# Performance work log

Measured on AMD Instinct MI355X. Metric: run time of the kernel, lower is better.

The kernel has to match this reference:

```python
import jax, jax.numpy as jnp
import numpy as np
from jax import lax

B, T, MEL, D, H, NC = 8, 256, 128, 192, 4, 20
C_EVENT, C_SCENE = 8, 64
ETA, LR, ALPHA = 0.9, 0.1, 0.01  # memory momentum, write lr, forget rate
EPS = 1e-5


def _ln(x, g, b):
    m = x.mean(-1, keepdims=True)
    v = ((x - m) ** 2).mean(-1, keepdims=True)
    return (x - m) / jnp.sqrt(v + EPS) * g + b


def _mem_step(x, t, M, S, Wk, Wv, Wq, chunk):
    # x: [B,D]; M,S: [B,D,D]. Titans-style neural memory, updated every `chunk` steps.
    k = x @ Wk
    v = x @ Wv
    q = x @ Wq
    err = v - jnp.einsum('bd,bde->be', k, M)          # surprise / prediction error
    S_new = ETA * S + LR * jnp.einsum('bd,be->bde', k, err)
    M_new = (1.0 - ALPHA) * M + S_new
    upd = (t % chunk) == 0
    S = jnp.where(upd, S_new, S)
    M = jnp.where(upd, M_new, M)
    out = jnp.einsum('bd,bde->be', q, M)              # retrieval
    return out, M, S


def setup_inputs() -> dict:
    key = jax.random.key(0)
    ks = jax.random.split(key, 24)
    w = lambda k, shp, s=0.05: jax.random.normal(k, shp, dtype=jnp.float32) * s
    inp = {
        'x': jax.random.normal(ks[0], (B, T, MEL), dtype=jnp.float32),
        'W_in': w(ks[1], (MEL, D)), 'b_in': jnp.zeros((D,), jnp.float32),
        # MHA at seq_len=1: softmax over one key -> weight 1, so only V and out proj matter
        'Wv_a': w(ks[2], (D, D)), 'bv_a': jnp.zeros((D,), jnp.float32),
        'Wo_a': w(ks[3], (D, D)), 'bo_a': jnp.zeros((D,), jnp.float32),
        # conformer conv module (degenerate seq_len=1: depthwise conv -> center tap)
        'ln1_g': jnp.ones((D,), jnp.float32), 'ln1_b': jnp.zeros((D,), jnp.float32),
        'pw1_w': w(ks[4], (D, 2 * D)), 'pw1_b': jnp.zeros((2 * D,), jnp.float32),
        'dw_w': w(ks[5], (D,), 0.2), 'dw_b': jnp.zeros((D,), jnp.float32),
        'bn_s': jnp.ones((D,), jnp.float32), 'bn_b': jnp.zeros((D,), jnp.float32),
        'pw2_w': w(ks[6], (D, D)), 'pw2_b': jnp.zeros((D,), jnp.float32),
        # theta (event) / delta (scene) neural memory projections
        'Wk_t': w(ks[7], (D, D)), 'Wv_t': w(ks[8], (D, D)), 'Wq_t': w(ks[9], (D, D)),
        'Wk_d': w(ks[10], (D, D)), 'Wv_d': w(ks[11], (D, D)), 'Wq_d': w(ks[12], (D, D)),
        'ln2_g': jnp.ones((D,), jnp.float32), 'ln2_b': jnp.zeros((D,), jnp.float32),
        'Wc': w(ks[13], (D, NC)), 'bc': jnp.zeros((NC,), jnp.float32),
    }
    return inp


def reference(x, W_in, b_in, Wv_a, bv_a, Wo_a, bo_a, ln1_g, ln1_b, pw1_w, pw1_b,
              dw_w, dw_b, bn_s, bn_b, pw2_w, pw2_b, Wk_t, Wv_t, Wq_t,
              Wk_d, Wv_d, Wq_d, ln2_g, ln2_b, Wc, bc):
    xp = x @ W_in + b_in                               # [B,T,D]

    def step(carry, inp):
        x_t, t = inp                                   # x_t: [B,D]
        Mt, St, Md, Sd = carry
        d_out, Md, Sd = _mem_step(x_t, t, Md, Sd, Wk_d, Wv_d, Wq_d, C_SCENE)
        x1 = x_t + 0.5 * d_out
        attn = (x1 @ Wv_a + bv_a) @ Wo_a + bo_a        # single-token self-attn
        x2 = x1 + attn
        h = _ln(x2, ln1_g, ln1_b)
        h = h @ pw1_w + pw1_b
        a, g = jnp.split(h, 2, axis=-1)
        h = a * jax.nn.sigmoid(g)                      # GLU
        h = h * dw_w + dw_b                            # depthwise conv center tap
        h = h * bn_s + bn_b                            # eval-mode BN
        h = jax.nn.silu(h)
        h = h @ pw2_w + pw2_b
        x3 = x2 + h
        t_out, Mt, St = _mem_step(x3, t, Mt, St, Wk_t, Wv_t, Wq_t, C_EVENT)
        x4 = x3 + 0.5 * t_out
        return (Mt, St, Md, Sd), _ln(x4, ln2_g, ln2_b)

    z = jnp.zeros((B, D, D), jnp.float32)
    xs = (jnp.swapaxes(xp, 0, 1), jnp.arange(T))       # [T,B,D], [T]
    _, ys = lax.scan(step, (z, z, z, z), xs)
    y = jnp.swapaxes(ys, 0, 1)                         # [B,T,D]
    pooled = y.mean(axis=1)
    return pooled @ Wc + bc                            # [B,NC]
```

## Files before the change

kernel.cpp:

```cpp
#include <hip/hip_runtime.h>
#include <math.h>

#define Bb 8
#define Tt 256
#define MEL 128
#define Dd 192
#define NCc 20
#define ND 4
#define NT 32
#define ETAc 0.9f
#define LRc 0.1f
#define MDEC 0.99f
#define EPSc 1e-5f
#define PT 4
#define RTT 8
#define PADD 196
#define UPAD 193

__device__ __forceinline__ float sigmoidf_(float x) {
    return 1.0f / (1.0f + __expf(-x));
}

__device__ __forceinline__ float memcoef(int n, int i) {
    float m = LRc, pw = LRc;
    for (int nn = i + 1; nn <= n; nn++) { pw *= ETAc; m = MDEC * m + pw; }
    return m;
}

__device__ __forceinline__ float dot4(float4 a, float4 b) {
    return a.x * b.x + a.y * b.y + a.z * b.z + a.w * b.w;
}

__global__ __launch_bounds__(192) void setup(
    const float* __restrict__ Wv_a, const float* __restrict__ Wo_a,
    const float* __restrict__ bv_a, const float* __restrict__ bo_a,
    const float* __restrict__ Wq_t, const float* __restrict__ Wq_d,
    const float* __restrict__ x, const float* __restrict__ W_in,
    const float* __restrict__ b_in, const float* __restrict__ Wk_d,
    const float* __restrict__ Wv_d,
    float* __restrict__ Wavo_ws, float* __restrict__ b_avo,
    float* __restrict__ WqtT, float* __restrict__ WqdT,
    float* __restrict__ Kd_ws, float* __restrict__ Vd_ws,
    float* __restrict__ pooled, unsigned int* __restrict__ ctr)
{
    __shared__ __align__(16) float smem[512];
    int blk = blockIdx.x, tid = threadIdx.x;

    if (blk < 192) {
        int m = blk;
        smem[tid] = Wv_a[m * Dd + tid];
        __syncthreads();
        int o = tid;
        float acc = 0.f;
        #pragma unroll 8
        for (int k = 0; k < Dd; k += 4) {
            acc += Wo_a[(k + 0) * Dd + o] * smem[k + 0];
            acc += Wo_a[(k + 1) * Dd + o] * smem[k + 1];
            acc += Wo_a[(k + 2) * Dd + o] * smem[k + 2];
            acc += Wo_a[(k + 3) * Dd + o] * smem[k + 3];
        }
        Wavo_ws[m * Dd + o] = acc;
        return;
    }
    if (blk == 192) {
        int o = tid;
        float s = bo_a[o];
        #pragma unroll 4
        for (int m = 0; m < Dd; m++) s += bv_a[m] * Wo_a[m * Dd + o];
        b_avo[o] = s;
        return;
    }
    if (blk < 241) {
        int r0 = 4 * (blk - 193);
        float4 v;
        v.x = Wq_t[(r0 + 0) * Dd + tid];
        v.y = Wq_t[(r0 + 1) * Dd + tid];
        v.z = Wq_t[(r0 + 2) * Dd + tid];
        v.w = Wq_t[(r0 + 3) * Dd + tid];
        *(float4*)&WqtT[tid * Dd + r0] = v;
        return;
    }
    if (blk < 289) {
        int r0 = 4 * (blk - 241);
        float4 v;
        v.x = Wq_d[(r0 + 0) * Dd + tid];
        v.y = Wq_d[(r0 + 1) * Dd + tid];
        v.z = Wq_d[(r0 + 2) * Dd + tid];
        v.w = Wq_d[(r0 + 3) * Dd + tid];
        *(float4*)&WqdT[tid * Dd + r0] = v;
        return;
    }
    if (blk == 289) {
        for (int q = tid; q < Bb * Dd; q += 192) pooled[q] = 0.f;
        if (tid == 0) *ctr = 0u;
        return;
    }

    int q = blk - 290;
    int b = q >> 2, i = q & 3;
    float* XR = smem;
    float* XP = smem + 128;
    if (tid < 128) XR[tid] = x[((size_t)b * Tt + 64 * i) * MEL + tid];
    __syncthreads();
    {
        int o = tid;
        float acc = b_in[o];
        #pragma unroll 8
        for (int k = 0; k < MEL; k += 4) {
            acc += W_in[(k + 0) * Dd + o] * XR[k + 0];
            acc += W_in[(k + 1) * Dd + o] * XR[k + 1];
            acc += W_in[(k + 2) * Dd + o] * XR[k + 2];
            acc += W_in[(k + 3) * Dd + o] * XR[k + 3];
        }
        XP[o] = acc;
    }
    __syncthreads();
    {
        int o = tid;
        float ak = 0.f, av = 0.f;
        #pragma unroll 4
        for (int k = 0; k < Dd; k += 4) {
            float x0 = XP[k + 0], x1 = XP[k + 1], x2 = XP[k + 2], x3 = XP[k + 3];
            ak += Wk_d[(k + 0) * Dd + o] * x0 + Wk_d[(k + 1) * Dd + o] * x1
                + Wk_d[(k + 2) * Dd + o] * x2 + Wk_d[(k + 3) * Dd + o] * x3;
            av += Wv_d[(k + 0) * Dd + o] * x0 + Wv_d[(k + 1) * Dd + o] * x1
                + Wv_d[(k + 2) * Dd + o] * x2 + Wv_d[(k + 3) * Dd + o] * x3;
        }
        Kd_ws[(b * ND + i) * Dd + o] = ak;
        Vd_ws[(b * ND + i) * Dd + o] = av;
    }
}

__global__ __launch_bounds__(192) void delta_solve(
    const float* __restrict__ WqdT, const float* __restrict__ Kd_ws,
    float* __restrict__ Vd_ws, float* __restrict__ Ud_ws)
{
    int blk = blockIdx.x, b = blk / 5, role = blk % 5, tid = threadIdx.x;
    if (role == 0) {
        __shared__ __align__(16) float K4[ND][Dd], V4[ND][Dd];
        __shared__ float G[16], mc[16];
        for (int q = tid; q < ND * 48; q += 192) {
            int i = q / 48, c = q - i * 48;
            ((float4*)K4[i])[c] = ((const float4*)&Kd_ws[(b * ND + i) * Dd])[c];
            ((float4*)V4[i])[c] = ((const float4*)&Vd_ws[(b * ND + i) * Dd])[c];
        }
        __syncthreads();
        if (tid < 16) {
            int i = tid >> 2, j = tid & 3;
            float s = 0.f;
            for (int d = 0; d < Dd; d++) s += K4[i][d] * K4[j][d];
            G[tid] = s;
            mc[tid] = (j <= i) ? memcoef(i, j) : 0.f;
        }
        __syncthreads();
        for (int i = 1; i < ND; i++) {
            float acc = V4[i][tid];
            for (int m = 0; m < i; m++)
                acc -= mc[(i - 1) * ND + m] * G[i * ND + m] * V4[m][tid];
            V4[i][tid] = acc;
        }
        for (int i = 0; i < ND; i++) Vd_ws[(b * ND + i) * Dd + tid] = V4[i][tid];
    } else {
        __shared__ float KS[Dd];
        int i = role - 1;
        KS[tid] = Kd_ws[(b * ND + i) * Dd + tid];
        __syncthreads();
        int o = tid;
        float acc = 0.f;
        #pragma unroll 8
        for (int k = 0; k < Dd; k += 4) {
            acc += WqdT[(k + 0) * Dd + o] * KS[k + 0];
            acc += WqdT[(k + 1) * Dd + o] * KS[k + 1];
            acc += WqdT[(k + 2) * Dd + o] * KS[k + 2];
            acc += WqdT[(k + 3) * Dd + o] * KS[k + 3];
        }
        Ud_ws[(b * ND + i) * Dd + o] = acc;
    }
}

__global__ __launch_bounds__(192) void pipeline(
    const float* __restrict__ x, const float* __restrict__ W_in,
    const float* __restrict__ b_in,
    const float* __restrict__ ln1_g, const float* __restrict__ ln1_b,
    const float* __restrict__ pw1_w, const float* __restrict__ pw1_b,
    const float* __restrict__ dw_w, const float* __restrict__ dw_b,
    const float* __restrict__ bn_s, const float* __restrict__ bn_b,
    const float* __restrict__ pw2_w, const float* __restrict__ pw2_b,
    const float* __restrict__ Wavo_ws, const float* __restrict__ b_avo,
    const float* __restrict__ Ed_ws, const float* __restrict__ Ud_ws,
    const float* __restrict__ Wk_t, const float* __restrict__ Wv_t,
    const float* __restrict__ WqtT,
    float* __restrict__ x3_ws, float* __restrict__ Kt_ws,
    float* __restrict__ Vt_ws, float* __restrict__ Ut_ws)
{
    int blk = blockIdx.x;
    int b = blk >> 6, tile = blk & 63;
    int t0 = tile * PT, n = tile >> 4;
    int tid = threadIdx.x;

    __shared__ __align__(16) float XR[PT][MEL];
    __shared__ __align__(16) float XP[PT][Dd];
    __shared__ __align__(16) float ED[ND][PADD], UD[ND][PADD];
    __shared__ __align__(16) float X1[PT][Dd], X2[PT][Dd];
    __shared__ __align__(16) float LNX[PT][Dd], HG[PT][Dd];
    __shared__ float X3row[Dd];
    __shared__ float KTs[Dd];
    __shared__ float WQs[PT * ND];
    __shared__ float mv[PT][2];

    if (tid < 128) {
        int r = tid >> 5, c = tid & 31;
        ((float4*)XR[r])[c] = ((const float4*)&x[((size_t)b * Tt + t0 + r) * MEL])[c];
    }
    for (int q = tid; q < ND * 48 * 2; q += 192) {
        int which = q >= ND * 48;
        int qq = which ? q - ND * 48 : q;
        int i = qq / 48, c = qq - i * 48;
        if (!which) ((float4*)ED[i])[c] = ((const float4*)&Ed_ws[(b * ND + i) * Dd])[c];
        else        ((float4*)UD[i])[c] = ((const float4*)&Ud_ws[(b * ND + i) * Dd])[c];
    }
    __syncthreads();

    int o = tid;
    {
        float acc[PT];
        float bb = b_in[o];
        #pragma unroll
        for (int r = 0; r < PT; r++) acc[r] = bb;
        #pragma unroll 8
        for (int k = 0; k < MEL; k += 4) {
            float w0 = W_in[(k + 0) * Dd + o], w1 = W_in[(k + 1) * Dd + o];
            float w2 = W_in[(k + 2) * Dd + o], w3 = W_in[(k + 3) * Dd + o];
            #pragma unroll
            for (int r = 0; r < PT; r++) {
                float4 xv = *(const float4*)&XR[r][k];
                acc[r] += w0 * xv.x + w1 * xv.y + w2 * xv.z + w3 * xv.w;
            }
        }
        #pragma unroll
        for (int r = 0; r < PT; r++) XP[r][tid] = acc[r];
    }
    __syncthreads();

    if (tid < 128) {
        int r = tid >> 5, i = (tid >> 3) & 3, c = tid & 7;
        float s = 0.f;
        const float* xp = XP[r];
        const float* u = UD[i];
        #pragma unroll
        for (int j = 0; j < 24; j++) s += xp[c * 24 + j] * u[c * 24 + j];
        s += __shfl_down(s, 4, 8);
        s += __shfl_down(s, 2, 8);
        s += __shfl_down(s, 1, 8);
        if (c == 0) {
            float coef = (i <= n) ? memcoef(n, i) : 0.f;
            WQs[r * ND + i] = s * coef;
        }
    }
    __syncthreads();

    {
        #pragma unroll
        for (int r = 0; r < PT; r++) {
            float dout = WQs[r * ND + 0] * ED[0][tid] + WQs[r * ND + 1] * ED[1][tid]
                       + WQs[r * ND + 2] * ED[2][tid] + WQs[r * ND + 3] * ED[3][tid];
            X1[r][tid] = XP[r][tid] + 0.5f * dout;
        }
    }
    __syncthreads();

    {
        float acc[PT];
        float bb = b_avo[o];
        #pragma unroll
        for (int r = 0; r < PT; r++) acc[r] = bb;
        #pragma unroll 8
        for (int k = 0; k < Dd; k += 4) {
            float w0 = Wavo_ws[(k + 0) * Dd + o], w1 = Wavo_ws[(k + 1) * Dd + o];
            float w2 = Wavo_ws[(k + 2) * Dd + o], w3 = Wavo_ws[(k + 3) * Dd + o];
            #pragma unroll
            for (int r = 0; r < PT; r++) {
                float4 xv = *(const float4*)&X1[r][k];
                acc[r] += w0 * xv.x + w1 * xv.y + w2 * xv.z + w3 * xv.w;
            }
        }
        #pragma unroll
        for (int r = 0; r < PT; r++) X2[r][tid] = X1[r][tid] + acc[r];
    }
    __syncthreads();

    if (tid < 128) {
        int r = tid >> 5, j = tid & 31;
        float s = 0.f, sq = 0.f;
        for (int d = j; d < Dd; d += 32) { float v = X2[r][d]; s += v; sq += v * v; }
        for (int off = 16; off > 0; off >>= 1) {
            s += __shfl_down(s, off, 32); sq += __shfl_down(sq, off, 32);
        }
        if (j == 0) {
            float mean = s / Dd;
            mv[r][0] = mean;
            mv[r][1] = rsqrtf(sq / Dd - mean * mean + EPSc);
        }
    }
    __syncthreads();
    {
        float g = ln1_g[tid], bb = ln1_b[tid];
        #pragma unroll
        for (int r = 0; r < PT; r++)
            LNX[r][tid] = (X2[r][tid] - mv[r][0]) * mv[r][1] * g + bb;
    }
    __syncthreads();

    {
        float aa[PT], gg[PT];
        float ba = pw1_b[o], bg = pw1_b[o + Dd];
        #pragma unroll
        for (int r = 0; r < PT; r++) { aa[r] = ba; gg[r] = bg; }
        #pragma unroll 4
        for (int k = 0; k < Dd; k += 4) {
            float wa0 = pw1_w[(k + 0) * 2 * Dd + o], wg0 = pw1_w[(k + 0) * 2 * Dd + Dd + o];
            float wa1 = pw1_w[(k + 1) * 2 * Dd + o], wg1 = pw1_w[(k + 1) * 2 * Dd + Dd + o];
            float wa2 = pw1_w[(k + 2) * 2 * Dd + o], wg2 = pw1_w[(k + 2) * 2 * Dd + Dd + o];
            float wa3 = pw1_w[(k + 3) * 2 * Dd + o], wg3 = pw1_w[(k + 3) * 2 * Dd + Dd + o];
            #pragma unroll
            for (int r = 0; r < PT; r++) {
                float4 xv = *(const float4*)&LNX[r][k];
                aa[r] += wa0 * xv.x + wa1 * xv.y + wa2 * xv.z + wa3 * xv.w;
                gg[r] += wg0 * xv.x + wg1 * xv.y + wg2 * xv.z + wg3 * xv.w;
            }
        }
        float dww = dw_w[o], dwb = dw_b[o], bns = bn_s[o], bnb = bn_b[o];
        #pragma unroll
        for (int r = 0; r < PT; r++) {
            float h = aa[r] * sigmoidf_(gg[r]);
            h = h * dww + dwb;
            h = h * bns + bnb;
            h = h * sigmoidf_(h);
            HG[r][tid] = h;
        }
    }
    __syncthreads();

    {
        float acc[PT];
        float bb = pw2_b[o];
        #pragma unroll
        for (int r = 0; r < PT; r++) acc[r] = bb;
        #pragma unroll 8
        for (int k = 0; k < Dd; k += 4) {
            float w0 = pw2_w[(k + 0) * Dd + o], w1 = pw2_w[(k + 1) * Dd + o];
            float w2 = pw2_w[(k + 2) * Dd + o], w3 = pw2_w[(k + 3) * Dd + o];
            #pragma unroll
            for (int r = 0; r < PT; r++) {
                float4 xv = *(const float4*)&HG[r][k];
                acc[r] += w0 * xv.x + w1 * xv.y + w2 * xv.z + w3 * xv.w;
            }
        }
        #pragma unroll
        for (int r = 0; r < PT; r++) {
            float v = X2[r][tid] + acc[r];
            if (r == 0) X3row[tid] = v;
            x3_ws[((size_t)b * Tt + t0 + r) * Dd + tid] = v;
        }
    }

    if ((tile & 1) == 0) {
        int i8 = tile >> 1;
        __syncthreads();
        {
            float ak = 0.f, av = 0.f;
            #pragma unroll 4
            for (int k = 0; k < Dd; k += 4) {
                float x0 = X3row[k + 0], x1v = X3row[k + 1];
                float x2v = X3row[k + 2], x3v = X3row[k + 3];
                ak += Wk_t[(k + 0) * Dd + o] * x0 + Wk_t[(k + 1) * Dd + o] * x1v
                    + Wk_t[(k + 2) * Dd + o] * x2v + Wk_t[(k + 3) * Dd + o] * x3v;
                av += Wv_t[(k + 0) * Dd + o] * x0 + Wv_t[(k + 1) * Dd + o] * x1v
                    + Wv_t[(k + 2) * Dd + o] * x2v + Wv_t[(k + 3) * Dd + o] * x3v;
            }
            Kt_ws[(b * NT + i8) * Dd + o] = ak;
            Vt_ws[(b * NT + i8) * Dd + o] = av;
            KTs[o] = ak;
        }
        __syncthreads();
        {
            float au = 0.f;
            #pragma unroll 8
            for (int k = 0; k < Dd; k += 4) {
                au += WqtT[(k + 0) * Dd + o] * KTs[k + 0]
                    + WqtT[(k + 1) * Dd + o] * KTs[k + 1]
                    + WqtT[(k + 2) * Dd + o] * KTs[k + 2]
                    + WqtT[(k + 3) * Dd + o] * KTs[k + 3];
            }
            Ut_ws[(b * NT + i8) * Dd + o] = au;
        }
    }
}

__global__ __launch_bounds__(192) void theta_solve(
    const float* __restrict__ Kt_ws, const float* __restrict__ Vt_ws,
    float* __restrict__ Et_ws)
{
    int b = blockIdx.x, tid = threadIdx.x;
    __shared__ __align__(16) float K[NT][PADD], V[NT][PADD];
    __shared__ float G[NT * NT], mcc[NT * NT];
    __shared__ float T[NT * 33];

    for (int q = tid; q < NT * 48; q += 192) {
        int i = q / 48, c = q - i * 48;
        ((float4*)K[i])[c] = ((const float4*)&Kt_ws[(b * NT + i) * Dd])[c];
        ((float4*)V[i])[c] = ((const float4*)&Vt_ws[(b * NT + i) * Dd])[c];
    }
    if (tid < NT) {
        int i = tid;
        float m = 0.f, pw = LRc;
        for (int nn = 0; nn < NT; nn++) {
            float v;
            if (nn < i) v = 0.f;
            else if (nn == i) { m = LRc; v = m; }
            else { pw *= ETAc; m = MDEC * m + pw; v = m; }
            mcc[nn * NT + i] = v;
        }
    }
    __syncthreads();
    for (int p = tid; p < NT * NT; p += 192) {
        int i = p >> 5, j = p & 31;
        const float4* ki = (const float4*)K[i];
        const float4* kj = (const float4*)K[j];
        float s = 0.f;
        #pragma unroll 4
        for (int kk = 0; kk < 48; kk++) s += dot4(ki[kk], kj[kk]);
        G[p] = s;
    }
    __syncthreads();
    for (int p = tid; p < NT * NT; p += 192) {
        int i = p >> 5, m = p & 31;
        G[p] = (m < i) ? mcc[(i - 1) * NT + m] * G[p] : 0.f;
    }
    __syncthreads();
    if (tid < NT) {
        int j = tid;
        T[j * 33 + j] = 1.f;
        for (int i = j + 1; i < NT; i++) {
            float s = 0.f;
            for (int m = j; m < i; m++) s += G[i * NT + m] * T[m * 33 + j];
            T[i * 33 + j] = -s;
        }
    }
    __syncthreads();
    {
        for (int i = 0; i < NT; i++) {
            float s = 0.f;
            for (int j = 0; j <= i; j++) s += T[i * 33 + j] * V[j][tid];
            Et_ws[(b * NT + i) * Dd + tid] = s;
        }
    }
}

__global__ __launch_bounds__(256) void retrieve(
    const float* __restrict__ x3_ws, const float* __restrict__ Ut_ws,
    const float* __restrict__ Et_ws, const float* __restrict__ ln2_g,
    const float* __restrict__ ln2_b, float* __restrict__ pooled,
    const float* __restrict__ Wc, const float* __restrict__ bc,
    float* __restrict__ out, unsigned int* __restrict__ ctr)
{
    int blk = blockIdx.x, b = blk >> 5, tile = blk & 31;
    int t0 = tile * RTT, n = tile;
    int tid = threadIdx.x;

    __shared__ float UT[NT][UPAD];
    __shared__ __align__(16) float XS[RTT][PADD];
    __shared__ float WQ[RTT * NT];
    __shared__ float mv[RTT][2];
    __shared__ float PLD[Bb * Dd];
    __shared__ bool isLast;

    for (int q = tid; q < NT * Dd; q += 256) {
        int i = q / Dd, c = q - i * Dd;
        UT[i][c] = Ut_ws[(size_t)b * NT * Dd + q];
    }
    for (int q = tid; q < RTT * 48; q += 256) {
        int r = q / 48, c = q - r * 48;
        ((float4*)XS[r])[c] = ((const float4*)&x3_ws[((size_t)b * Tt + t0 + r) * Dd])[c];
    }
    __syncthreads();

    {
        int r = tid >> 5, i = tid & 31;
        const float* u = UT[i];
        const float* xr = XS[r];
        float s = 0.f;
        #pragma unroll 8
        for (int kk = 0; kk < Dd; kk++) s += u[kk] * xr[kk];
        float coef = (i <= n) ? memcoef(n, i) : 0.f;
        WQ[tid] = s * coef;
    }
    __syncthreads();

    if (tid < Dd) {
        float acc[RTT] = {};
        #pragma unroll 4
        for (int i = 0; i < NT; i++) {
            float e = Et_ws[(b * NT + i) * Dd + tid];
            #pragma unroll
            for (int r = 0; r < RTT; r++) acc[r] += WQ[r * NT + i] * e;
        }
        #pragma unroll
        for (int r = 0; r < RTT; r++) XS[r][tid] += 0.5f * acc[r];
    }
    __syncthreads();

    {
        int r = tid >> 5, j = tid & 31;
        float s = 0.f, sq = 0.f;
        for (int d = j; d < Dd; d += 32) { float v = XS[r][d]; s += v; sq += v * v; }
        for (int off = 16; off > 0; off >>= 1) {
            s += __shfl_down(s, off, 32); sq += __shfl_down(sq, off, 32);
        }
        if (j == 0) {
            float mean = s / Dd;
            mv[r][0] = mean;
            mv[r][1] = rsqrtf(sq / Dd - mean * mean + EPSc);
        }
    }
    __syncthreads();

    if (tid < Dd) {
        float g = ln2_g[tid], bb = ln2_b[tid];
        float sum = 0.f;
        #pragma unroll
        for (int r = 0; r < RTT; r++)
            sum += (XS[r][tid] - mv[r][0]) * mv[r][1] * g + bb;
        atomicAdd(&pooled[b * Dd + tid], sum);
    }

    __threadfence();
    if (tid == 0) {
        unsigned int old = atomicAdd(ctr, 1u);
        isLast = (old == (unsigned)(Bb * 32 - 1));
    }
    __syncthreads();
    if (isLast) {
        __threadfence();
        for (int q = tid; q < Bb * Dd; q += 256)
            PLD[q] = *(volatile const float*)&pooled[q];
        __syncthreads();
        if (tid < Bb * NCc) {
            int bo = tid / NCc, c = tid - bo * NCc;
            float s = 0.f;
            for (int d = 0; d < Dd; d++) s += PLD[bo * Dd + d] * Wc[d * NCc + c];
            out[tid] = s * (1.0f / Tt) + bc[c];
        }
    }
}

extern "C" void kernel_launch(void* const* d_in, const int* in_sizes, int n_in,
                              void* d_out, int out_size, void* d_ws, size_t ws_size,
                              hipStream_t stream) {
    const float* x     = (const float*)d_in[0];
    const float* W_in  = (const float*)d_in[1];
    const float* b_in  = (const float*)d_in[2];
    const float* Wv_a  = (const float*)d_in[3];
    const float* bv_a  = (const float*)d_in[4];
    const float* Wo_a  = (const float*)d_in[5];
    const float* bo_a  = (const float*)d_in[6];
    const float* ln1_g = (const float*)d_in[7];
    const float* ln1_b = (const float*)d_in[8];
    const float* pw1_w = (const float*)d_in[9];
    const float* pw1_b = (const float*)d_in[10];
    const float* dw_w  = (const float*)d_in[11];
    const float* dw_b  = (const float*)d_in[12];
    const float* bn_s  = (const float*)d_in[13];
    const float* bn_b  = (const float*)d_in[14];
    const float* pw2_w = (const float*)d_in[15];
    const float* pw2_b = (const float*)d_in[16];
    const float* Wk_t  = (const float*)d_in[17];
    const float* Wv_t  = (const float*)d_in[18];
    const float* Wq_t  = (const float*)d_in[19];
    const float* Wk_d  = (const float*)d_in[20];
    const float* Wv_d  = (const float*)d_in[21];
    const float* Wq_d  = (const float*)d_in[22];
    const float* ln2_g = (const float*)d_in[23];
    const float* ln2_b = (const float*)d_in[24];
    const float* Wc    = (const float*)d_in[25];
    const float* bc    = (const float*)d_in[26];

    float* ws = (float*)d_ws;
    size_t off = 0;
    float* x3_ws   = ws + off; off += (size_t)Bb * Tt * Dd;
    float* Kd_ws   = ws + off; off += Bb * ND * Dd;
    float* Vd_ws   = ws + off; off += Bb * ND * Dd;
    float* Ud_ws   = ws + off; off += Bb * ND * Dd;
    float* Kt_ws   = ws + off; off += Bb * NT * Dd;
    float* Vt_ws   = ws + off; off += Bb * NT * Dd;
    float* Et_ws   = ws + off; off += Bb * NT * Dd;
    float* Ut_ws   = ws + off; off += Bb * NT * Dd;
    float* pooled  = ws + off; off += Bb * Dd;
    float* Wavo_ws = ws + off; off += Dd * Dd;
    float* WqtT    = ws + off; off += Dd * Dd;
    float* WqdT    = ws + off; off += Dd * Dd;
    float* b_avo   = ws + off; off += Dd;
    unsigned int* ctr = (unsigned int*)(ws + off); off += 1;

    setup<<<322, 192, 0, stream>>>(
        Wv_a, Wo_a, bv_a, bo_a, Wq_t, Wq_d,
        x, W_in, b_in, Wk_d, Wv_d,
        Wavo_ws, b_avo, WqtT, WqdT, Kd_ws, Vd_ws, pooled, ctr);
    delta_solve<<<Bb * 5, 192, 0, stream>>>(WqdT, Kd_ws, Vd_ws, Ud_ws);
    pipeline<<<Bb * 64, 192, 0, stream>>>(
        x, W_in, b_in, ln1_g, ln1_b, pw1_w, pw1_b, dw_w, dw_b,
        bn_s, bn_b, pw2_w, pw2_b, Wavo_ws, b_avo, Vd_ws, Ud_ws,
        Wk_t, Wv_t, WqtT, x3_ws, Kt_ws, Vt_ws, Ut_ws);
    theta_solve<<<Bb, 192, 0, stream>>>(Kt_ws, Vt_ws, Et_ws);
    retrieve<<<Bb * 32, 256, 0, stream>>>(
        x3_ws, Ut_ws, Et_ws, ln2_g, ln2_b, pooled, Wc, bc, (float*)d_out, ctr);
}
```

Baseline: 224.7 us.

## Fold delta and theta solves into preceding kernels via last-block atomic counters

Removes the separate delta_solve and theta_solve launches. The last-arriving block of setup, and the last block per batch of pipeline, now does the solve work using atomic counters and threadfences. The Ut projection moves from per-tile pipeline blocks into the theta solve block as a batched 32-row matmul, and pipeline shared memory is unioned. This cuts launch overhead and dependency gaps, but serializes the delta solve for all 8 batches onto one block and adds a hipMemsetAsync for the counters.

```diff
diff --git a/kernel.cpp b/kernel.cpp
--- a/kernel.cpp
+++ b/kernel.cpp
@@ -41,36 +41,39 @@
     float* __restrict__ Wavo_ws, float* __restrict__ b_avo,
     float* __restrict__ WqtT, float* __restrict__ WqdT,
     float* __restrict__ Kd_ws, float* __restrict__ Vd_ws,
-    float* __restrict__ pooled, unsigned int* __restrict__ ctr)
+    float* __restrict__ Ud_ws,
+    float* __restrict__ pooled, unsigned int* __restrict__ ctrs)
 {
-    __shared__ __align__(16) float smem[512];
+    __shared__ __align__(16) float scol[Dd];
+    __shared__ __align__(16) float XR[MEL];
+    __shared__ __align__(16) float XPs[Dd];
+    __shared__ __align__(16) float TK[ND][Dd], TV[ND][Dd];
+    __shared__ float TG[16], TMC[16];
+    __shared__ bool lastFlag;
+
     int blk = blockIdx.x, tid = threadIdx.x;
 
     if (blk < 192) {
         int m = blk;
-        smem[tid] = Wv_a[m * Dd + tid];
+        scol[tid] = Wv_a[m * Dd + tid];
         __syncthreads();
         int o = tid;
         float acc = 0.f;
         #pragma unroll 8
         for (int k = 0; k < Dd; k += 4) {
-            acc += Wo_a[(k + 0) * Dd + o] * smem[k + 0];
-            acc += Wo_a[(k + 1) * Dd + o] * smem[k + 1];
-            acc += Wo_a[(k + 2) * Dd + o] * smem[k + 2];
-            acc += Wo_a[(k + 3) * Dd + o] * smem[k + 3];
+            acc += Wo_a[(k + 0) * Dd + o] * scol[k + 0];
+            acc += Wo_a[(k + 1) * Dd + o] * scol[k + 1];
+            acc += Wo_a[(k + 2) * Dd + o] * scol[k + 2];
+            acc += Wo_a[(k + 3) * Dd + o] * scol[k + 3];
         }
         Wavo_ws[m * Dd + o] = acc;
-        return;
-    }
-    if (blk == 192) {
+    } else if (blk == 192) {
         int o = tid;
         float s = bo_a[o];
         #pragma unroll 4
         for (int m = 0; m < Dd; m++) s += bv_a[m] * Wo_a[m * Dd + o];
         b_avo[o] = s;
-        return;
-    }
-    if (blk < 241) {
+    } else if (blk < 241) {
         int r0 = 4 * (blk - 193);
         float4 v;
         v.x = Wq_t[(r0 + 0) * Dd + tid];
@@ -78,9 +81,7 @@
         v.z = Wq_t[(r0 + 2) * Dd + tid];
         v.w = Wq_t[(r0 + 3) * Dd + tid];
         *(float4*)&WqtT[tid * Dd + r0] = v;
-        return;
-    }
-    if (blk < 289) {
+    } else if (blk < 289) {
         int r0 = 4 * (blk - 241);
         float4 v;
         v.x = Wq_d[(r0 + 0) * Dd + tid];
@@ -88,95 +89,105 @@
         v.z = Wq_d[(r0 + 2) * Dd + tid];
         v.w = Wq_d[(r0 + 3) * Dd + tid];
         *(float4*)&WqdT[tid * Dd + r0] = v;
-        return;
-    }
-    if (blk == 289) {
+    } else if (blk == 289) {
         for (int q = tid; q < Bb * Dd; q += 192) pooled[q] = 0.f;
-        if (tid == 0) *ctr = 0u;
-        return;
-    }
-
-    int q = blk - 290;
-    int b = q >> 2, i = q & 3;
-    float* XR = smem;
-    float* XP = smem + 128;
-    if (tid < 128) XR[tid] = x[((size_t)b * Tt + 64 * i) * MEL + tid];
-    __syncthreads();
-    {
-        int o = tid;
-        float acc = b_in[o];
-        #pragma unroll 8
-        for (int k = 0; k < MEL; k += 4) {
-            acc += W_in[(k + 0) * Dd + o] * XR[k + 0];
-            acc += W_in[(k + 1) * Dd + o] * XR[k + 1];
-            acc += W_in[(k + 2) * Dd + o] * XR[k + 2];
-            acc += W_in[(k + 3) * Dd + o] * XR[k + 3];
-        }
-        XP[o] = acc;
-    }
-    __syncthreads();
-    {
-        int o = tid;
-        float ak = 0.f, av = 0.f;
-        #pragma unroll 4
-        for (int k = 0; k < Dd; k += 4) {
-            float x0 = XP[k + 0], x1 = XP[k + 1], x2 = XP[k + 2], x3 = XP[k + 3];
-            ak += Wk_d[(k + 0) * Dd + o] * x0 + Wk_d[(k + 1) * Dd + o] * x1
-                + Wk_d[(k + 2) * Dd + o] * x2 + Wk_d[(k + 3) * Dd + o] * x3;
-            av += Wv_d[(k + 0) * Dd + o] * x0 + Wv_d[(k + 1) * Dd + o] * x1
-                + Wv_d[(k + 2) * Dd + o] * x2 + Wv_d[(k + 3) * Dd + o] * x3;
-        }
-        Kd_ws[(b * ND + i) * Dd + o] = ak;
-        Vd_ws[(b * ND + i) * Dd + o] = av;
-    }
-}
-
-__global__ __launch_bounds__(192) void delta_solve(
-    const float* __restrict__ WqdT, const float* __restrict__ Kd_ws,
-    float* __restrict__ Vd_ws, float* __restrict__ Ud_ws)
-{
-    int blk = blockIdx.x, b = blk / 5, role = blk % 5, tid = threadIdx.x;
-    if (role == 0) {
-        __shared__ __align__(16) float K4[ND][Dd], V4[ND][Dd];
-        __shared__ float G[16], mc[16];
-        for (int q = tid; q < ND * 48; q += 192) {
-            int i = q / 48, c = q - i * 48;
-            ((float4*)K4[i])[c] = ((const float4*)&Kd_ws[(b * ND + i) * Dd])[c];
-            ((float4*)V4[i])[c] = ((const float4*)&Vd_ws[(b * ND + i) * Dd])[c];
+    } else {
+        int q = blk - 290;
+        int b = q >> 2, i = q & 3;
+        if (tid < 128) XR[tid] = x[((size_t)b * Tt + 64 * i) * MEL + tid];
+        __syncthreads();
+        {
+            int o = tid;
+            float acc = b_in[o];
+            #pragma unroll 8
+            for (int k = 0; k < MEL; k += 4) {
+                acc += W_in[(k + 0) * Dd + o] * XR[k + 0];
+                acc += W_in[(k + 1) * Dd + o] * XR[k + 1];
+                acc += W_in[(k + 2) * Dd + o] * XR[k + 2];
+                acc += W_in[(k + 3) * Dd + o] * XR[k + 3];
+            }
+            XPs[o] = acc;
+        }
+        __syncthreads();
+        {
+            int o = tid;
+            float ak = 0.f, av = 0.f;
+            #pragma unroll 4
+            for (int k = 0; k < Dd; k += 4) {
+                float x0 = XPs[k + 0], x1 = XPs[k + 1], x2 = XPs[k + 2], x3 = XPs[k + 3];
+                ak += Wk_d[(k + 0) * Dd + o] * x0 + Wk_d[(k + 1) * Dd + o] * x1
+                    + Wk_d[(k + 2) * Dd + o] * x2 + Wk_d[(k + 3) * Dd + o] * x3;
+                av += Wv_d[(k + 0) * Dd + o] * x0 + Wv_d[(k + 1) * Dd + o] * x1
+                    + Wv_d[(k + 2) * Dd + o] * x2 + Wv_d[(k + 3) * Dd + o] * x3;
+            }
+            Kd_ws[(b * ND + i) * Dd + o] = ak;
+            Vd_ws[(b * ND + i) * Dd + o] = av;
+        }
+    }
+
+    __threadfence();
+    __syncthreads();
+    if (tid == 0) lastFlag = (atomicAdd(&ctrs[0], 1u) == 321u);
+    __syncthreads();
+    if (!lastFlag) return;
+    __threadfence();
+
+    for (int b = 0; b < Bb; b++) {
+        for (int q = tid; q < ND * Dd; q += 192) {
+            int i = q / Dd, c = q - i * Dd;
+            TK[i][c] = ((volatile const float*)Kd_ws)[(size_t)b * ND * Dd + q];
+            TV[i][c] = ((volatile const float*)Vd_ws)[(size_t)b * ND * Dd + q];
         }
         __syncthreads();
         if (tid < 16) {
             int i = tid >> 2, j = tid & 3;
             float s = 0.f;
-            for (int d = 0; d < Dd; d++) s += K4[i][d] * K4[j][d];
-            G[tid] = s;
-            mc[tid] = (j <= i) ? memcoef(i, j) : 0.f;
+            for (int d = 0; d < Dd; d++) s += TK[i][d] * TK[j][d];
+            TG[tid] = s;
+            TMC[tid] = (j <= i) ? memcoef(i, j) : 0.f;
         }
         __syncthreads();
-        for (int i = 1; i < ND; i++) {
-            float acc = V4[i][tid];
-            for (int m = 0; m < i; m++)
-                acc -= mc[(i - 1) * ND + m] * G[i * ND + m] * V4[m][tid];
-            V4[i][tid] = acc;
-        }
-        for (int i = 0; i < ND; i++) Vd_ws[(b * ND + i) * Dd + tid] = V4[i][tid];
-    } else {
-        __shared__ float KS[Dd];
-        int i = role - 1;
-        KS[tid] = Kd_ws[(b * ND + i) * Dd + tid];
+        {
+            for (int i = 1; i < ND; i++) {
+                float acc = TV[i][tid];
+                for (int m = 0; m < i; m++)
+                    acc -= TMC[(i - 1) * ND + m] * TG[i * ND + m] * TV[m][tid];
+                TV[i][tid] = acc;
+            }
+            for (int i = 0; i < ND; i++) Vd_ws[(b * ND + i) * Dd + tid] = TV[i][tid];
+            float u0 = 0.f, u1 = 0.f, u2 = 0.f, u3 = 0.f;
+            #pragma unroll 4
+            for (int e = 0; e < Dd; e++) {
+                float w = ((volatile const float*)WqdT)[e * Dd + tid];
+                u0 += w * TK[0][e]; u1 += w * TK[1][e];
+                u2 += w * TK[2][e]; u3 += w * TK[3][e];
+            }
+            Ud_ws[(b * ND + 0) * Dd + tid] = u0;
+            Ud_ws[(b * ND + 1) * Dd + tid] = u1;
+            Ud_ws[(b * ND + 2) * Dd + tid] = u2;
+            Ud_ws[(b * ND + 3) * Dd + tid] = u3;
+        }
         __syncthreads();
-        int o = tid;
-        float acc = 0.f;
-        #pragma unroll 8
-        for (int k = 0; k < Dd; k += 4) {
-            acc += WqdT[(k + 0) * Dd + o] * KS[k + 0];
-            acc += WqdT[(k + 1) * Dd + o] * KS[k + 1];
-            acc += WqdT[(k + 2) * Dd + o] * KS[k + 2];
-            acc += WqdT[(k + 3) * Dd + o] * KS[k + 3];
-        }
-        Ud_ws[(b * ND + i) * Dd + o] = acc;
     }
 }
+
+union PipeLDS {
+    struct {
+        float XR[PT][MEL];
+        float XP[PT][Dd];
+        float ED[ND][PADD], UD[ND][PADD];
+        float X1[PT][Dd], X2[PT][Dd];
+        float LNX[PT][Dd], HG[PT][Dd];
+        float X3row[Dd];
+        float WQs[PT * ND];
+        float mv[PT][2];
+    } p;
+    struct {
+        float K[NT][PADD], V[NT][PADD];
+        float G[NT * NT], mcc[NT * NT];
+        float T[NT * 33];
+    } s;
+};
 
 __global__ __launch_bounds__(192) void pipeline(
     const float* __restrict__ x, const float* __restrict__ W_in,
@@ -191,33 +202,27 @@
     const float* __restrict__ Wk_t, const float* __restrict__ Wv_t,
     const float* __restrict__ WqtT,
     float* __restrict__ x3_ws, float* __restrict__ Kt_ws,
-    float* __restrict__ Vt_ws, float* __restrict__ Ut_ws)
+    float* __restrict__ Vt_ws, float* __restrict__ Et_ws,
+    float* __restrict__ Ut_ws, unsigned int* __restrict__ ctrs)
 {
+    __shared__ PipeLDS U;
+    __shared__ bool doSolve;
+
     int blk = blockIdx.x;
     int b = blk >> 6, tile = blk & 63;
     int t0 = tile * PT, n = tile >> 4;
     int tid = threadIdx.x;
 
-    __shared__ __align__(16) float XR[PT][MEL];
-    __shared__ __align__(16) float XP[PT][Dd];
-    __shared__ __align__(16) float ED[ND][PADD], UD[ND][PADD];
-    __shared__ __align__(16) float X1[PT][Dd], X2[PT][Dd];
-    __shared__ __align__(16) float LNX[PT][Dd], HG[PT][Dd];
-    __shared__ float X3row[Dd];
-    __shared__ float KTs[Dd];
-    __shared__ float WQs[PT * ND];
-    __shared__ float mv[PT][2];
-
     if (tid < 128) {
         int r = tid >> 5, c = tid & 31;
-        ((float4*)XR[r])[c] = ((const float4*)&x[((size_t)b * Tt + t0 + r) * MEL])[c];
+        ((float4*)U.p.XR[r])[c] = ((const float4*)&x[((size_t)b * Tt + t0 + r) * MEL])[c];
     }
     for (int q = tid; q < ND * 48 * 2; q += 192) {
         int which = q >= ND * 48;
         int qq = which ? q - ND * 48 : q;
         int i = qq / 48, c = qq - i * 48;
-        if (!which) ((float4*)ED[i])[c] = ((const float4*)&Ed_ws[(b * ND + i) * Dd])[c];
-        else        ((float4*)UD[i])[c] = ((const float4*)&Ud_ws[(b * ND + i) * Dd])[c];
+        if (!which) ((float4*)U.p.ED[i])[c] = ((const float4*)&Ed_ws[(b * ND + i) * Dd])[c];
+        else        ((float4*)U.p.UD[i])[c] = ((const float4*)&Ud_ws[(b * ND + i) * Dd])[c];
     }
     __syncthreads();
 
@@ -233,20 +238,20 @@
             float w2 = W_in[(k + 2) * Dd + o], w3 = W_in[(k + 3) * Dd + o];
             #pragma unroll
             for (int r = 0; r < PT; r++) {
-                float4 xv = *(const float4*)&XR[r][k];
+                float4 xv = *(const float4*)&U.p.XR[r][k];
                 acc[r] += w0 * xv.x + w1 * xv.y + w2 * xv.z + w3 * xv.w;
             }
         }
         #pragma unroll
-        for (int r = 0; r < PT; r++) XP[r][tid] = acc[r];
+        for (int r = 0; r < PT; r++) U.p.XP[r][tid] = acc[r];
     }
     __syncthreads();
 
     if (tid < 128) {
         int r = tid >> 5, i = (tid >> 3) & 3, c = tid & 7;
         float s = 0.f;
-        const float* xp = XP[r];
-        const float* u = UD[i];
+        const float* xp = U.p.XP[r];
+        const float* u = U.p.UD[i];
         #pragma unroll
         for (int j = 0; j < 24; j++) s += xp[c * 24 + j] * u[c * 24 + j];
         s += __shfl_down(s, 4, 8);
@@ -254,7 +259,7 @@
         s += __shfl_down(s, 1, 8);
         if (c == 0) {
             float coef = (i <= n) ? memcoef(n, i) : 0.f;
-            WQs[r * ND + i] = s * coef;
+            U.p.WQs[r * ND + i] = s * coef;
         }
     }
     __syncthreads();
@@ -262,9 +267,9 @@
     {
         #pragma unroll
         for (int r = 0; r < PT; r++) {
-            float dout = WQs[r * ND + 0] * ED[0][tid] + WQs[r * ND + 1] * ED[1][tid]
-                       + WQs[r * ND + 2] * ED[2][tid] + WQs[r * ND + 3] * ED[3][tid];
-            X1[r][tid] = XP[r][tid] + 0.5f * dout;
+            float dout = U.p.WQs[r * ND + 0] * U.p.ED[0][tid] + U.p.WQs[r * ND + 1] * U.p.ED[1][tid]
+                       + U.p.WQs[r * ND + 2] * U.p.ED[2][tid] + U.p.WQs[r * ND + 3] * U.p.ED[3][tid];
+            U.p.X1[r][tid] = U.p.XP[r][tid] + 0.5f * dout;
         }
     }
     __syncthreads();
@@ -280,26 +285,26 @@
             float w2 = Wavo_ws[(k + 2) * Dd + o], w3 = Wavo_ws[(k + 3) * Dd + o];
             #pragma unroll
             for (int r = 0; r < PT; r++) {
-                float4 xv = *(const float4*)&X1[r][k];
+                float4 xv = *(const float4*)&U.p.X1[r][k];
                 acc[r] += w0 * xv.x + w1 * xv.y + w2 * xv.z + w3 * xv.w;
             }
         }
         #pragma unroll
-        for (int r = 0; r < PT; r++) X2[r][tid] = X1[r][tid] + acc[r];
+        for (int r = 0; r < PT; r++) U.p.X2[r][tid] = U.p.X1[r][tid] + acc[r];
     }
     __syncthreads();
 
     if (tid < 128) {
         int r = tid >> 5, j = tid & 31;
         float s = 0.f, sq = 0.f;
-        for (int d = j; d < Dd; d += 32) { float v = X2[r][d]; s += v; sq += v * v; }
+        for (int d = j; d < Dd; d += 32) { float v = U.p.X2[r][d]; s += v; sq += v * v; }
         for (int off = 16; off > 0; off >>= 1) {
             s += __shfl_down(s, off, 32); sq += __shfl_down(sq, off, 32);
         }
         if (j == 0) {
             float mean = s / Dd;
-            mv[r][0] = mean;
-            mv[r][1] = rsqrtf(sq / Dd - mean * mean + EPSc);
+            U.p.mv[r][0] = mean;
+            U.p.mv[r][1] = rsqrtf(sq / Dd - mean * mean + EPSc);
         }
     }
     __syncthreads();
@@ -307,7 +312,7 @@
         float g = ln1_g[tid], bb = ln1_b[tid];
         #pragma unroll
         for (int r = 0; r < PT; r++)
-            LNX[r][tid] = (X2[r][tid] - mv[r][0]) * mv[r][1] * g + bb;
+            U.p.LNX[r][tid] = (U.p.X2[r][tid] - U.p.mv[r][0]) * U.p.mv[r][1] * g + bb;
     }
     __syncthreads();
 
@@ -324,7 +329,7 @@
             float wa3 = pw1_w[(k + 3) * 2 * Dd + o], wg3 = pw1_w[(k + 3) * 2 * Dd + Dd + o];
             #pragma unroll
             for (int r = 0; r < PT; r++) {
-                float4 xv = *(const float4*)&LNX[r][k];
+                float4 xv = *(const float4*)&U.p.LNX[r][k];
                 aa[r] += wa0 * xv.x + wa1 * xv.y + wa2 * xv.z + wa3 * xv.w;
                 gg[r] += wg0 * xv.x + wg1 * xv.y + wg2 * xv.z + wg3 * xv.w;
             }
@@ -336,7 +341,7 @@
             h = h * dww + dwb;
             h = h * bns + bnb;
             h = h * sigmoidf_(h);
-            HG[r][tid] = h;
+            U.p.HG[r][tid] = h;
         }
     }
     __syncthreads();
@@ -352,14 +357,14 @@
             float w2 = pw2_w[(k + 2) * Dd + o], w3 = pw2_w[(k + 3) * Dd + o];
             #pragma unroll
             for (int r = 0; r < PT; r++) {
-                float4 xv = *(const float4*)&HG[r][k];
+                float4 xv = *(const float4*)&U.p.HG[r][k];
                 acc[r] += w0 * xv.x + w1 * xv.y + w2 * xv.z + w3 * xv.w;
             }
         }
         #pragma unroll
         for (int r = 0; r < PT; r++) {
-            float v = X2[r][tid] + acc[r];
-            if (r == 0) X3row[tid] = v;
+            float v = U.p.X2[r][tid] + acc[r];
+            if (r == 0) U.p.X3row[tid] = v;
             x3_ws[((size_t)b * Tt + t0 + r) * Dd + tid] = v;
         }
     }
@@ -367,49 +372,31 @@
     if ((tile & 1) == 0) {
         int i8 = tile >> 1;
         __syncthreads();
-        {
-            float ak = 0.f, av = 0.f;
-            #pragma unroll 4
-            for (int k = 0; k < Dd; k += 4) {
-                float x0 = X3row[k + 0], x1v = X3row[k + 1];
-                float x2v = X3row[k + 2], x3v = X3row[k + 3];
-                ak += Wk_t[(k + 0) * Dd + o] * x0 + Wk_t[(k + 1) * Dd + o] * x1v
-                    + Wk_t[(k + 2) * Dd + o] * x2v + Wk_t[(k + 3) * Dd + o] * x3v;
-                av += Wv_t[(k + 0) * Dd + o] * x0 + Wv_t[(k + 1) * Dd + o] * x1v
-                    + Wv_t[(k + 2) * Dd + o] * x2v + Wv_t[(k + 3) * Dd + o] * x3v;
-            }
-            Kt_ws[(b * NT + i8) * Dd + o] = ak;
-            Vt_ws[(b * NT + i8) * Dd + o] = av;
-            KTs[o] = ak;
-        }
-        __syncthreads();
-        {
-            float au = 0.f;
-            #pragma unroll 8
-            for (int k = 0; k < Dd; k += 4) {
-                au += WqtT[(k + 0) * Dd + o] * KTs[k + 0]
-                    + WqtT[(k + 1) * Dd + o] * KTs[k + 1]
-                    + WqtT[(k + 2) * Dd + o] * KTs[k + 2]
-                    + WqtT[(k + 3) * Dd + o] * KTs[k + 3];
-            }
-            Ut_ws[(b * NT + i8) * Dd + o] = au;
-        }
-    }
-}
-
-__global__ __launch_bounds__(192) void theta_solve(
-    const float* __restrict__ Kt_ws, const float* __restrict__ Vt_ws,
-    float* __restrict__ Et_ws)
-{
-    int b = blockIdx.x, tid = threadIdx.x;
-    __shared__ __align__(16) float K[NT][PADD], V[NT][PADD];
-    __shared__ float G[NT * NT], mcc[NT * NT];
-    __shared__ float T[NT * 33];
-
-    for (int q = tid; q < NT * 48; q += 192) {
-        int i = q / 48, c = q - i * 48;
-        ((float4*)K[i])[c] = ((const float4*)&Kt_ws[(b * NT + i) * Dd])[c];
-        ((float4*)V[i])[c] = ((const float4*)&Vt_ws[(b * NT + i) * Dd])[c];
+        float ak = 0.f, av = 0.f;
+        #pragma unroll 4
+        for (int k = 0; k < Dd; k += 4) {
+            float x0 = U.p.X3row[k + 0], x1v = U.p.X3row[k + 1];
+            float x2v = U.p.X3row[k + 2], x3v = U.p.X3row[k + 3];
+            ak += Wk_t[(k + 0) * Dd + o] * x0 + Wk_t[(k + 1) * Dd + o] * x1v
+                + Wk_t[(k + 2) * Dd + o] * x2v + Wk_t[(k + 3) * Dd + o] * x3v;
+            av += Wv_t[(k + 0) * Dd + o] * x0 + Wv_t[(k + 1) * Dd + o] * x1v
+                + Wv_t[(k + 2) * Dd + o] * x2v + Wv_t[(k + 3) * Dd + o] * x3v;
+        }
+        Kt_ws[(b * NT + i8) * Dd + o] = ak;
+        Vt_ws[(b * NT + i8) * Dd + o] = av;
+    }
+
+    __threadfence();
+    __syncthreads();
+    if (tid == 0) doSolve = (atomicAdd(&ctrs[1 + b], 1u) == 63u);
+    __syncthreads();
+    if (!doSolve) return;
+    __threadfence();
+
+    for (int q = tid; q < NT * Dd; q += 192) {
+        int i = q / Dd, c = q - i * Dd;
+        U.s.K[i][c] = ((volatile const float*)Kt_ws)[(size_t)b * NT * Dd + q];
+        U.s.V[i][c] = ((volatile const float*)Vt_ws)[(size_t)b * NT * Dd + q];
     }
     if (tid < NT) {
         int i = tid;
@@ -419,41 +406,58 @@
             if (nn < i) v = 0.f;
             else if (nn == i) { m = LRc; v = m; }
             else { pw *= ETAc; m = MDEC * m + pw; v = m; }
-            mcc[nn * NT + i] = v;
+            U.s.mcc[nn * NT + i] = v;
         }
     }
     __syncthreads();
     for (int p = tid; p < NT * NT; p += 192) {
         int i = p >> 5, j = p & 31;
-        const float4* ki = (const float4*)K[i];
-        const float4* kj = (const float4*)K[j];
+        const float4* ki = (const float4*)U.s.K[i];
+        const float4* kj = (const float4*)U.s.K[j];
         float s = 0.f;
         #pragma unroll 4
         for (int kk = 0; kk < 48; kk++) s += dot4(ki[kk], kj[kk]);
-        G[p] = s;
+        U.s.G[p] = s;
     }
     __syncthreads();
     for (int p = tid; p < NT * NT; p += 192) {
         int i = p >> 5, m = p & 31;
-        G[p] = (m < i) ? mcc[(i - 1) * NT + m] * G[p] : 0.f;
+        U.s.G[p] = (m < i) ? U.s.mcc[(i - 1) * NT + m] * U.s.G[p] : 0.f;
     }
     __syncthreads();
     if (tid < NT) {
         int j = tid;
-        T[j * 33 + j] = 1.f;
+        U.s.T[j * 33 + j] = 1.f;
         for (int i = j + 1; i < NT; i++) {
             float s = 0.f;
-            for (int m = j; m < i; m++) s += G[i * NT + m] * T[m * 33 + j];
-            T[i * 33 + j] = -s;
+            for (int m = j; m < i; m++) s += U.s.G[i * NT + m] * U.s.T[m * 33 + j];
+            U.s.T[i * 33 + j] = -s;
         }
     }
     __syncthreads();
     {
         for (int i = 0; i < NT; i++) {
             float s = 0.f;
-            for (int j = 0; j <= i; j++) s += T[i * 33 + j] * V[j][tid];
+            for (int j = 0; j <= i; j++) s += U.s.T[i * 33 + j] * U.s.V[j][tid];
             Et_ws[(b * NT + i) * Dd + tid] = s;
         }
+    }
+    for (int half = 0; half < 2; half++) {
+        float acc[16];
+        #pragma unroll
+        for (int i = 0; i < 16; i++) acc[i] = 0.f;
+        for (int e = 0; e < Dd; e += 4) {
+            float w0 = WqtT[(e + 0) * Dd + tid], w1 = WqtT[(e + 1) * Dd + tid];
+            float w2 = WqtT[(e + 2) * Dd + tid], w3 = WqtT[(e + 3) * Dd + tid];
+            #pragma unroll
+            for (int i = 0; i < 16; i++) {
+                float4 kv = *(const float4*)&U.s.K[half * 16 + i][e];
+                acc[i] += w0 * kv.x + w1 * kv.y + w2 * kv.z + w3 * kv.w;
+            }
+        }
+        #pragma unroll
+        for (int i = 0; i < 16; i++)
+            Ut_ws[(b * NT + half * 16 + i) * Dd + tid] = acc[i];
     }
 }
 
@@ -462,7 +466,7 @@
     const float* __restrict__ Et_ws, const float* __restrict__ ln2_g,
     const float* __restrict__ ln2_b, float* __restrict__ pooled,
     const float* __restrict__ Wc, const float* __restrict__ bc,
-    float* __restrict__ out, unsigned int* __restrict__ ctr)
+    float* __restrict__ out, unsigned int* __restrict__ ctrs)
 {
     int blk = blockIdx.x, b = blk >> 5, tile = blk & 31;
     int t0 = tile * RTT, n = tile;
@@ -535,22 +539,19 @@
     }
 
     __threadfence();
-    if (tid == 0) {
-        unsigned int old = atomicAdd(ctr, 1u);
-        isLast = (old == (unsigned)(Bb * 32 - 1));
-    }
-    __syncthreads();
-    if (isLast) {
-        __threadfence();
-        for (int q = tid; q < Bb * Dd; q += 256)
-            PLD[q] = *(volatile const float*)&pooled[q];
-        __syncthreads();
-        if (tid < Bb * NCc) {
-            int bo = tid / NCc, c = tid - bo * NCc;
-            float s = 0.f;
-            for (int d = 0; d < Dd; d++) s += PLD[bo * Dd + d] * Wc[d * NCc + c];
-            out[tid] = s * (1.0f / Tt) + bc[c];
-        }
+    __syncthreads();
+    if (tid == 0) isLast = (atomicAdd(&ctrs[9], 1u) == (unsigned)(Bb * 32 - 1));
+    __syncthreads();
+    if (!isLast) return;
+    __threadfence();
+    for (int q = tid; q < Bb * Dd; q += 256)
+        PLD[q] = *(volatile const float*)&pooled[q];
+    __syncthreads();
+    if (tid < Bb * NCc) {
+        int bo = tid / NCc, c = tid - bo * NCc;
+        float s = 0.f;
+        for (int d = 0; d < Dd; d++) s += PLD[bo * Dd + d] * Wc[d * NCc + c];
+        out[tid] = s * (1.0f / Tt) + bc[c];
     }
 }
 
@@ -600,18 +601,18 @@
     float* WqtT    = ws + off; off += Dd * Dd;
     float* WqdT    = ws + off; off += Dd * Dd;
     float* b_avo   = ws + off; off += Dd;
-    unsigned int* ctr = (unsigned int*)(ws + off); off += 1;
+    unsigned int* ctrs = (unsigned int*)(ws + off); off += 16;
+
+    hipMemsetAsync(ctrs, 0, 16 * sizeof(unsigned int), stream);
 
     setup<<<322, 192, 0, stream>>>(
         Wv_a, Wo_a, bv_a, bo_a, Wq_t, Wq_d,
         x, W_in, b_in, Wk_d, Wv_d,
-        Wavo_ws, b_avo, WqtT, WqdT, Kd_ws, Vd_ws, pooled, ctr);
-    delta_solve<<<Bb * 5, 192, 0, stream>>>(WqdT, Kd_ws, Vd_ws, Ud_ws);
+        Wavo_ws, b_avo, WqtT, WqdT, Kd_ws, Vd_ws, Ud_ws, pooled, ctrs);
     pipeline<<<Bb * 64, 192, 0, stream>>>(
         x, W_in, b_in, ln1_g, ln1_b, pw1_w, pw1_b, dw_w, dw_b,
         bn_s, bn_b, pw2_w, pw2_b, Wavo_ws, b_avo, Vd_ws, Ud_ws,
-        Wk_t, Wv_t, WqtT, x3_ws, Kt_ws, Vt_ws, Ut_ws);
-    theta_solve<<<Bb, 192, 0, stream>>>(Kt_ws, Vt_ws, Et_ws);
+        Wk_t, Wv_t, WqtT, x3_ws, Kt_ws, Vt_ws, Et_ws, Ut_ws, ctrs);
     retrieve<<<Bb * 32, 256, 0, stream>>>(
-        x3_ws, Ut_ws, Et_ws, ln2_g, ln2_b, pooled, Wc, bc, (float*)d_out, ctr);
+        x3_ws, Ut_ws, Et_ws, ln2_g, ln2_b, pooled, Wc, bc, (float*)d_out, ctrs);
 }
```

Result: slower. 550.7 us (+145.1%).
